# Optimization experiments

Measured on AMD Instinct MI355X. Metric: run time of the kernel, lower is better.

The kernel has to match this reference:

```python
import jax, jax.numpy as jnp
import numpy as np

N_TOKENS = 131072      # flattened batch of latents
EMBED_DIM = 64         # embedding_dim
NUM_CODES = 1024       # num_embeddings
COMMIT_COST = 0.25     # commitment_cost
EPS_NORM = 1e-12       # F.normalize eps


def _l2_normalize(x):
    # matches F.normalize(x, dim=1): x / max(||x||_2, eps)
    n = jnp.sqrt(jnp.sum(x * x, axis=1, keepdims=True))
    return x / jnp.maximum(n, EPS_NORM)


def setup_inputs() -> dict:
    key = jax.random.key(0)
    k_in, k_w = jax.random.split(key)
    inputs = jax.random.normal(k_in, (N_TOKENS, EMBED_DIM), dtype=jnp.float32)
    # codebook init: uniform(-1/K, 1/K), as in the torch module
    weight = jax.random.uniform(k_w, (NUM_CODES, EMBED_DIM), dtype=jnp.float32,
                                minval=-1.0 / NUM_CODES, maxval=1.0 / NUM_CODES)
    return {"inputs": inputs, "weight": weight}


def reference(inputs, weight):
    # Eval-mode forward of VectorQuantizer (EMA/anchor update is a training-only
    # in-place buffer mutation and is excluded from the functional reference).
    input_shape = inputs.shape
    d = weight.shape[1]
    flat = inputs.reshape(-1, d)                         # [N, D]

    normed_z = _l2_normalize(jax.lax.stop_gradient(flat))  # [N, D]
    normed_cb = _l2_normalize(weight)                       # [K, D]
    # distances = -cosine similarity; argmin picks closest code
    distances = -jnp.einsum('nd,kd->nk', normed_z, normed_cb)  # [N, K]
    idx = jnp.argmin(distances, axis=1)                         # [N]

    encodings = jax.nn.one_hot(idx, weight.shape[0], dtype=jnp.float32)  # [N, K]
    # one-hot @ weight == gather of codebook rows
    quantized = jnp.take(weight, idx, axis=0).reshape(input_shape)

    e_latent_loss = jnp.mean((jax.lax.stop_gradient(quantized) - inputs) ** 2)
    q_latent_loss = jnp.mean((quantized - jax.lax.stop_gradient(inputs)) ** 2)
    loss = q_latent_loss + COMMIT_COST * e_latent_loss

    # straight-through estimator
    quantized_st = inputs + jax.lax.stop_gradient(quantized - inputs)

    avg_probs = jnp.mean(encodings, axis=0)  # [K]
    perplexity = jnp.exp(-jnp.sum(avg_probs * jnp.log(avg_probs + 1e-10)))

    return loss, quantized_st, perplexity, encodings
```

## Files before the change

### kernel.cpp

```cpp
#include <hip/hip_runtime.h>
#include <math.h>

#define N_TOK 131072
#define DIM 64
#define KCODES 1024
#define TPB 128
#define TIE_EPS 1e-4f

typedef __attribute__((ext_vector_type(8))) short short8;
typedef __attribute__((ext_vector_type(4))) float float4v;

static __device__ inline unsigned short f2bf(float x) {
    unsigned u = __float_as_uint(x);
    unsigned r = (u + 0x7FFF + ((u >> 16) & 1)) >> 16;
    return (unsigned short)r;
}
static __device__ inline float bf2f(unsigned short b) {
    return __uint_as_float(((unsigned)b) << 16);
}

__global__ __launch_bounds__(64) void vq_prep(
    const float* __restrict__ w, unsigned short* __restrict__ bfrag_hi,
    unsigned short* __restrict__ bfrag_lo, double* __restrict__ inv_n64,
    float* __restrict__ nw, int* __restrict__ count, int* __restrict__ nflag,
    double* __restrict__ delta)
{
    int k = blockIdx.x;
    int d = threadIdx.x;
    float v = w[k * DIM + d];
    float s = v * v;
    #pragma unroll
    for (int off = 32; off; off >>= 1) s += __shfl_xor(s, off);
    float den = fmaxf(sqrtf(s), 1e-12f);
    float nv = v / den;
    unsigned short hi = f2bf(nv);
    unsigned short lo = f2bf(nv - bf2f(hi));

    int t  = k >> 4;
    int nl = k & 15;
    int s2 = d >> 5;
    int q  = (d >> 3) & 3;
    int j  = d & 7;
    int l  = nl + 16 * q;
    size_t pos = ((size_t)(t * 2 + s2) * 64 + l) * 8 + j;
    bfrag_hi[pos] = hi;
    bfrag_lo[pos] = lo;

    double vd = (double)v;
    double sd = vd * vd;
    #pragma unroll
    for (int off = 32; off; off >>= 1) sd += __shfl_xor(sd, off);
    if (d == 0) {
        inv_n64[k] = 1.0 / fmax(sqrt(sd), 1e-12);
        nw[k] = den;
    }
    if (k == 0) {
        for (int i = d; i < KCODES; i += 64) count[i] = 0;
        if (d == 0) { nflag[0] = 0; delta[0] = 0.0; }
    }
}

static __device__ inline void merge3(float& b, float& s, int& i, float ob, float os, int oi) {
    if (ob > b) { s = fmaxf(b, os); b = ob; i = oi; }
    else if (ob == b) { s = b; if (oi < i) i = oi; }
    else { s = fmaxf(s, ob); }
}

__global__ __launch_bounds__(256, 4) void vq_main(
    const float* __restrict__ inputs, const float* __restrict__ w,
    const unsigned short* __restrict__ bfrag_hi, const unsigned short* __restrict__ bfrag_lo,
    const float* __restrict__ nw, int* __restrict__ g_idx, int* __restrict__ count,
    double* __restrict__ partial, int* __restrict__ nflag, int* __restrict__ flags,
    float* __restrict__ out_q, float* __restrict__ out_enc)
{
    __shared__ int   s_idx[TPB];
    __shared__ float s_part[4];

    const int tid  = threadIdx.x;
    const int lane = tid & 63;
    const int wv   = tid >> 6;
    const int col  = lane & 15;
    const int quad = lane >> 4;
    const int n0   = blockIdx.x * TPB;

    short8 ah[2][2], al[2][2];
    float n2z[2];
    #pragma unroll
    for (int s = 0; s < 2; s++) {
        int m = n0 + wv * 32 + s * 16 + col;
        const float* zp = inputs + (size_t)m * DIM + quad * 8;
        float4 f0 = *(const float4*)zp;
        float4 f1 = *(const float4*)(zp + 4);
        float4 f2 = *(const float4*)(zp + 32);
        float4 f3 = *(const float4*)(zp + 36);
        float v[16] = {f0.x,f0.y,f0.z,f0.w, f1.x,f1.y,f1.z,f1.w,
                       f2.x,f2.y,f2.z,f2.w, f3.x,f3.y,f3.z,f3.w};
        float ss = 0.f;
        #pragma unroll
        for (int j = 0; j < 16; j++) ss += v[j] * v[j];
        ss += __shfl_xor(ss, 16);
        ss += __shfl_xor(ss, 32);
        n2z[s] = ss;
        float inv = 1.0f / fmaxf(sqrtf(ss), 1e-12f);
        #pragma unroll
        for (int j = 0; j < 8; j++) {
            float x0 = v[j] * inv;
            unsigned short h0 = f2bf(x0);
            ah[s][0][j] = (short)h0;
            al[s][0][j] = (short)f2bf(x0 - bf2f(h0));
            float x1 = v[8 + j] * inv;
            unsigned short h1 = f2bf(x1);
            ah[s][1][j] = (short)h1;
            al[s][1][j] = (short)f2bf(x1 - bf2f(h1));
        }
    }

    float* enc0 = out_enc + (size_t)n0 * KCODES;
    float* zp4  = enc0 + 2 + tid * 4;
    const float4 zero4 = {0.f, 0.f, 0.f, 0.f};

    float best[8], sec[8]; int bidx[8];
    #pragma unroll
    for (int i = 0; i < 8; i++) { best[i] = -1e30f; sec[i] = -1e30f; bidx[i] = 0x7fffffff; }

    const short8* bhp = (const short8*)bfrag_hi;
    const short8* blp = (const short8*)bfrag_lo;
    short8 c0h = bhp[lane], c1h = bhp[64 + lane];
    short8 c0l = blp[lane], c1l = blp[64 + lane];

    for (int t = 0; t < 64; t++) {
        int tn = (t < 63) ? (t + 1) : 63;
        size_t o = (size_t)(2 * tn) * 64 + lane;
        short8 p0h = bhp[o], p1h = bhp[o + 64];
        short8 p0l = blp[o], p1l = blp[o + 64];

        if (t < 63) {
            *(float4*)zp4 = zero4;
            *(float4*)(zp4 + KCODES) = zero4;
            zp4 += 2 * KCODES;
        }

        float4v acc0 = {0.f,0.f,0.f,0.f}, acc1 = {0.f,0.f,0.f,0.f};
        acc0 = __builtin_amdgcn_mfma_f32_16x16x32_bf16(ah[0][0], c0h, acc0, 0,0,0);
        acc1 = __builtin_amdgcn_mfma_f32_16x16x32_bf16(ah[1][0], c0h, acc1, 0,0,0);
        acc0 = __builtin_amdgcn_mfma_f32_16x16x32_bf16(al[0][0], c0h, acc0, 0,0,0);
        acc1 = __builtin_amdgcn_mfma_f32_16x16x32_bf16(al[1][0], c0h, acc1, 0,0,0);
        acc0 = __builtin_amdgcn_mfma_f32_16x16x32_bf16(ah[0][0], c0l, acc0, 0,0,0);
        acc1 = __builtin_amdgcn_mfma_f32_16x16x32_bf16(ah[1][0], c0l, acc1, 0,0,0);
        acc0 = __builtin_amdgcn_mfma_f32_16x16x32_bf16(ah[0][1], c1h, acc0, 0,0,0);
        acc1 = __builtin_amdgcn_mfma_f32_16x16x32_bf16(ah[1][1], c1h, acc1, 0,0,0);
        acc0 = __builtin_amdgcn_mfma_f32_16x16x32_bf16(al[0][1], c1h, acc0, 0,0,0);
        acc1 = __builtin_amdgcn_mfma_f32_16x16x32_bf16(al[1][1], c1h, acc1, 0,0,0);
        acc0 = __builtin_amdgcn_mfma_f32_16x16x32_bf16(ah[0][1], c1l, acc0, 0,0,0);
        acc1 = __builtin_amdgcn_mfma_f32_16x16x32_bf16(ah[1][1], c1l, acc1, 0,0,0);

        int k = t * 16 + col;
        #pragma unroll
        for (int i = 0; i < 4; i++) {
            float v0 = acc0[i];
            sec[i]  = __builtin_amdgcn_fmed3f(best[i], sec[i], v0);
            bool g0 = v0 > best[i];
            best[i] = fmaxf(best[i], v0);
            bidx[i] = g0 ? k : bidx[i];
            float v1 = acc1[i];
            sec[4+i]  = __builtin_amdgcn_fmed3f(best[4+i], sec[4+i], v1);
            bool g1 = v1 > best[4 + i];
            best[4 + i] = fmaxf(best[4 + i], v1);
            bidx[4 + i] = g1 ? k : bidx[4 + i];
        }
        c0h = p0h; c1h = p1h; c0l = p0l; c1l = p1l;
    }

    #pragma unroll
    for (int i = 126; i < 128; i++) {
        int q = i * 256 + tid;
        if (q < 32767) *(float4*)(enc0 + 2 + 4 * (size_t)q) = zero4;
    }
    if (tid == 0) {
        *(float2*)enc0 = make_float2(0.f, 0.f);
        *(float2*)(enc0 + (size_t)TPB * KCODES - 2) = make_float2(0.f, 0.f);
    }

    #pragma unroll
    for (int off = 1; off < 16; off <<= 1) {
        #pragma unroll
        for (int i = 0; i < 8; i++) {
            float ob = __shfl_xor(best[i], off);
            float os = __shfl_xor(sec[i], off);
            int   oi = __shfl_xor(bidx[i], off);
            merge3(best[i], sec[i], bidx[i], ob, os, oi);
        }
    }

    float lsum = 0.f;
    #pragma unroll
    for (int s = 0; s < 2; s++) {
        #pragma unroll
        for (int i = 0; i < 4; i++) {
            int r = s * 4 + i;
            float n2 = __shfl(n2z[s], quad * 4 + i);
            if (col == 0) {
                int u  = quad * 4 + i;
                int tl = wv * 32 + s * 16 + u;
                int k  = bidx[r];
                s_idx[tl] = k;
                g_idx[n0 + tl] = k;
                atomicAdd(&count[k], 1);
                if (best[r] - sec[r] < TIE_EPS) {
                    int p = atomicAdd(nflag, 1);
                    flags[p] = n0 + tl;
                }
                float nwk = nw[k];
                float zw  = best[r] * sqrtf(n2) * nwk;
                lsum += n2 - 2.f * zw + nwk * nwk;
            }
        }
    }
    lsum += __shfl_xor(lsum, 16);
    lsum += __shfl_xor(lsum, 32);
    if (lane == 0) s_part[wv] = lsum;
    __syncthreads();
    if (tid == 0)
        partial[blockIdx.x] = (double)(s_part[0] + s_part[1] + s_part[2] + s_part[3]);

    if (tid < TPB)
        out_enc[(size_t)(n0 + tid) * KCODES + s_idx[tid]] = 1.0f;

    const size_t qbase = (size_t)n0 * DIM;
    #pragma unroll 4
    for (int i2 = 0; i2 < 32; i2++) {
        int p = i2 * 256 + tid;
        int r = p >> 6, c = p & 63;
        int k = s_idx[r];
        out_q[qbase + p] = w[(size_t)k * DIM + c];
    }
}

__global__ __launch_bounds__(64) void vq_rescan(
    const float* __restrict__ inputs, const float* __restrict__ w,
    const double* __restrict__ inv_n64, const int* __restrict__ g_idx,
    const int* __restrict__ flags, const int* __restrict__ nflag,
    int* __restrict__ count, float* __restrict__ out_q,
    float* __restrict__ out_enc, double* __restrict__ delta)
{
    __shared__ double sz[64];
    int lane = threadIdx.x;
    int nf = nflag[0];
    for (int i = blockIdx.x; i < nf; i += gridDim.x) {
        int tok = flags[i];
        double zd = (double)inputs[(size_t)tok * DIM + lane];
        double ss = zd * zd;
        #pragma unroll
        for (int off = 32; off; off >>= 1) ss += __shfl_xor(ss, off);
        sz[lane] = zd / fmax(sqrt(ss), 1e-12);
        __syncthreads();
        double bv = -1e300; int bi = 0x7fffffff;
        for (int c = 0; c < 16; c++) {
            int k = c * 64 + lane;
            double invk = inv_n64[k];
            double dot = 0.0;
            #pragma unroll 8
            for (int d = 0; d < DIM; d++)
                dot += sz[d] * ((double)w[(size_t)k * DIM + d] * invk);
            if (dot > bv) { bv = dot; bi = k; }
        }
        #pragma unroll
        for (int off = 1; off < 64; off <<= 1) {
            double ov = __shfl_xor(bv, off);
            int   oi = __shfl_xor(bi, off);
            if (ov > bv || (ov == bv && oi < bi)) { bv = ov; bi = oi; }
        }
        int kold = g_idx[tok];
        if (bi != kold) {
            double wn = (double)w[(size_t)bi * DIM + lane];
            double wo = (double)w[(size_t)kold * DIM + lane];
            double zr = (double)inputs[(size_t)tok * DIM + lane];
            double a = wn * wn - wo * wo - 2.0 * zr * (wn - wo);
            #pragma unroll
            for (int off = 32; off; off >>= 1) a += __shfl_xor(a, off);
            out_q[(size_t)tok * DIM + lane] = (float)wn;
            if (lane == 0) {
                atomicAdd(&count[kold], -1);
                atomicAdd(&count[bi], 1);
                out_enc[(size_t)tok * KCODES + kold] = 0.f;
                out_enc[(size_t)tok * KCODES + bi]   = 1.f;
                atomicAdd(delta, a);
            }
        }
        __syncthreads();
    }
}

__global__ __launch_bounds__(256) void vq_final(
    const int* __restrict__ count, const double* __restrict__ partial,
    const double* __restrict__ delta, float* __restrict__ out_loss,
    float* __restrict__ out_perp)
{
    __shared__ double s1[256], s2[256];
    int tid = threadIdx.x;
    double lp = 0.0, ls = 0.0;
    for (int k = tid; k < KCODES; k += 256) {
        double p = (double)count[k] / (double)N_TOK;
        lp += p * log(p + 1e-10);
    }
    for (int i = tid; i < 1024; i += 256) ls += partial[i];
    s1[tid] = lp; s2[tid] = ls;
    __syncthreads();
    for (int st = 128; st; st >>= 1) {
        if (tid < st) { s1[tid] += s1[tid + st]; s2[tid] += s2[tid + st]; }
        __syncthreads();
    }
    if (tid == 0) {
        out_perp[0] = (float)exp(-s1[0]);
        out_loss[0] = (float)(1.25 * (s2[0] + delta[0]) / ((double)N_TOK * (double)DIM));
    }
}

extern "C" void kernel_launch(void* const* d_in, const int* in_sizes, int n_in,
                              void* d_out, int out_size, void* d_ws, size_t ws_size,
                              hipStream_t stream) {
    const float* inputs = (const float*)d_in[0];
    const float* weight = (const float*)d_in[1];
    float* out      = (float*)d_out;
    float* out_loss = out;
    float* out_q    = out + 1;
    float* out_perp = out + 1 + (size_t)N_TOK * DIM;
    float* out_enc  = out_perp + 1;

    char* ws = (char*)d_ws;
    unsigned short* bfrag_hi = (unsigned short*)ws;
    unsigned short* bfrag_lo = (unsigned short*)(ws + 131072);
    double* inv_n64 = (double*)(ws + 262144);
    float*  nw      = (float*)(ws + 270336);
    int*    g_idx   = (int*)(ws + 274432);
    int*    count   = (int*)(ws + 798720);
    double* partial = (double*)(ws + 802816);
    double* delta   = (double*)(ws + 811008);
    int*    nflag   = (int*)(ws + 811016);
    int*    flags   = (int*)(ws + 811020);

    vq_prep<<<KCODES, 64, 0, stream>>>(weight, bfrag_hi, bfrag_lo, inv_n64, nw,
                                       count, nflag, delta);
    vq_main<<<N_TOK / TPB, 256, 0, stream>>>(inputs, weight, bfrag_hi, bfrag_lo, nw,
                                             g_idx, count, partial, nflag, flags,
                                             out_q, out_enc);
    vq_rescan<<<256, 64, 0, stream>>>(inputs, weight, inv_n64, g_idx, flags, nflag,
                                      count, out_q, out_enc, delta);
    vq_final<<<1, 256, 0, stream>>>(count, partial, delta, out_loss, out_perp);
}
```

Baseline: 679.4 us.

## Split encodings zero-fill and quantized gather out of the main VQ kernel

Moves the 512 MB one-hot zero-fill out of the MFMA argmin kernel into a separate grid-stride zeroing kernel. The one-hot writes and the codebook-row gather for the quantized output move into a new scatter kernel that reads the stored indices. The aim is to stop the bandwidth-bound stores from interleaving with the compute loop and to let each phase run at its own efficiency. The cost is two extra launches and an extra read of g_idx, and the compute no longer overlaps the memory writes.

After: 790.8 us. +16.4%, slower.

```diff
diff --git a/kernel.cpp b/kernel.cpp
--- a/kernel.cpp
+++ b/kernel.cpp
@@ -60,6 +60,21 @@
     }
 }
 
+__global__ __launch_bounds__(256) void vq_zero(float* __restrict__ enc)
+{
+    const size_t NF4 = ((size_t)N_TOK * KCODES - 4) / 4;
+    float4* p = (float4*)(enc + 2);
+    const float4 z4 = {0.f, 0.f, 0.f, 0.f};
+    size_t i = (size_t)blockIdx.x * 256 + threadIdx.x;
+    const size_t stride = (size_t)gridDim.x * 256;
+    for (size_t j = i; j < NF4; j += stride) p[j] = z4;
+    if (i == 0) {
+        enc[0] = 0.f; enc[1] = 0.f;
+        enc[(size_t)N_TOK * KCODES - 2] = 0.f;
+        enc[(size_t)N_TOK * KCODES - 1] = 0.f;
+    }
+}
+
 static __device__ inline void merge3(float& b, float& s, int& i, float ob, float os, int oi) {
     if (ob > b) { s = fmaxf(b, os); b = ob; i = oi; }
     else if (ob == b) { s = b; if (oi < i) i = oi; }
@@ -67,13 +82,11 @@
 }
 
 __global__ __launch_bounds__(256, 4) void vq_main(
-    const float* __restrict__ inputs, const float* __restrict__ w,
+    const float* __restrict__ inputs,
     const unsigned short* __restrict__ bfrag_hi, const unsigned short* __restrict__ bfrag_lo,
     const float* __restrict__ nw, int* __restrict__ g_idx, int* __restrict__ count,
-    double* __restrict__ partial, int* __restrict__ nflag, int* __restrict__ flags,
-    float* __restrict__ out_q, float* __restrict__ out_enc)
-{
-    __shared__ int   s_idx[TPB];
+    double* __restrict__ partial, int* __restrict__ nflag, int* __restrict__ flags)
+{
     __shared__ float s_part[4];
 
     const int tid  = threadIdx.x;
@@ -115,10 +128,6 @@
         }
     }
 
-    float* enc0 = out_enc + (size_t)n0 * KCODES;
-    float* zp4  = enc0 + 2 + tid * 4;
-    const float4 zero4 = {0.f, 0.f, 0.f, 0.f};
-
     float best[8], sec[8]; int bidx[8];
     #pragma unroll
     for (int i = 0; i < 8; i++) { best[i] = -1e30f; sec[i] = -1e30f; bidx[i] = 0x7fffffff; }
@@ -133,12 +142,6 @@
         size_t o = (size_t)(2 * tn) * 64 + lane;
         short8 p0h = bhp[o], p1h = bhp[o + 64];
         short8 p0l = blp[o], p1l = blp[o + 64];
-
-        if (t < 63) {
-            *(float4*)zp4 = zero4;
-            *(float4*)(zp4 + KCODES) = zero4;
-            zp4 += 2 * KCODES;
-        }
 
         float4v acc0 = {0.f,0.f,0.f,0.f}, acc1 = {0.f,0.f,0.f,0.f};
         acc0 = __builtin_amdgcn_mfma_f32_16x16x32_bf16(ah[0][0], c0h, acc0, 0,0,0);
@@ -172,16 +175,6 @@
     }
 
     #pragma unroll
-    for (int i = 126; i < 128; i++) {
-        int q = i * 256 + tid;
-        if (q < 32767) *(float4*)(enc0 + 2 + 4 * (size_t)q) = zero4;
-    }
-    if (tid == 0) {
-        *(float2*)enc0 = make_float2(0.f, 0.f);
-        *(float2*)(enc0 + (size_t)TPB * KCODES - 2) = make_float2(0.f, 0.f);
-    }
-
-    #pragma unroll
     for (int off = 1; off < 16; off <<= 1) {
         #pragma unroll
         for (int i = 0; i < 8; i++) {
@@ -200,10 +193,8 @@
             int r = s * 4 + i;
             float n2 = __shfl(n2z[s], quad * 4 + i);
             if (col == 0) {
-                int u  = quad * 4 + i;
-                int tl = wv * 32 + s * 16 + u;
+                int tl = wv * 32 + s * 16 + quad * 4 + i;
                 int k  = bidx[r];
-                s_idx[tl] = k;
                 g_idx[n0 + tl] = k;
                 atomicAdd(&count[k], 1);
                 if (best[r] - sec[r] < TIE_EPS) {
@@ -222,18 +213,20 @@
     __syncthreads();
     if (tid == 0)
         partial[blockIdx.x] = (double)(s_part[0] + s_part[1] + s_part[2] + s_part[3]);
-
-    if (tid < TPB)
-        out_enc[(size_t)(n0 + tid) * KCODES + s_idx[tid]] = 1.0f;
-
-    const size_t qbase = (size_t)n0 * DIM;
-    #pragma unroll 4
-    for (int i2 = 0; i2 < 32; i2++) {
-        int p = i2 * 256 + tid;
-        int r = p >> 6, c = p & 63;
-        int k = s_idx[r];
-        out_q[qbase + p] = w[(size_t)k * DIM + c];
-    }
+}
+
+__global__ __launch_bounds__(256) void vq_scatter(
+    const float* __restrict__ w, const int* __restrict__ g_idx,
+    float* __restrict__ out_q, float* __restrict__ out_enc)
+{
+    int g  = blockIdx.x * 256 + threadIdx.x;
+    int n  = g >> 4;
+    int d4 = (g & 15) * 4;
+    int k  = g_idx[n];
+    float4 q = *(const float4*)&w[(size_t)k * DIM + d4];
+    size_t ob = (size_t)n * DIM + d4;
+    out_q[ob + 0] = q.x; out_q[ob + 1] = q.y; out_q[ob + 2] = q.z; out_q[ob + 3] = q.w;
+    if ((g & 15) == 0) out_enc[(size_t)n * KCODES + k] = 1.0f;
 }
 
 __global__ __launch_bounds__(64) void vq_rescan(
@@ -341,9 +334,10 @@
 
     vq_prep<<<KCODES, 64, 0, stream>>>(weight, bfrag_hi, bfrag_lo, inv_n64, nw,
                                        count, nflag, delta);
-    vq_main<<<N_TOK / TPB, 256, 0, stream>>>(inputs, weight, bfrag_hi, bfrag_lo, nw,
-                                             g_idx, count, partial, nflag, flags,
-                                             out_q, out_enc);
+    vq_zero<<<2048, 256, 0, stream>>>(out_enc);
+    vq_main<<<N_TOK / TPB, 256, 0, stream>>>(inputs, bfrag_hi, bfrag_lo, nw,
+                                             g_idx, count, partial, nflag, flags);
+    vq_scatter<<<(N_TOK * 16) / 256, 256, 0, stream>>>(weight, g_idx, out_q, out_enc);
     vq_rescan<<<256, 64, 0, stream>>>(inputs, weight, inv_n64, g_idx, flags, nflag,
                                       count, out_q, out_enc, delta);
     vq_final<<<1, 256, 0, stream>>>(count, partial, delta, out_loss, out_perp);
```

## Front-load one-hot zero stores, split rescan dot accumulators, widen rescan grid

Applied to the files above, without the earlier changes.

Moves a quarter of the one-hot encoding zero-fill ahead of the MFMA loop, overlapping it with input loads and normalization. The remaining zero stores are spread over the first 48 iterations instead of 63, and the tail fix-up is adjusted to match. The rescan kernel's double-precision dot product is split into four independent accumulators to shorten the dependency chain, and its grid grows from 256 to 2048 blocks. This front-loads store traffic and adds more blocks in the rescan pass, at the cost of extra launch and scheduling overhead when few tokens are flagged.

Result: no change. 675.3 us (-0.6%).

```diff
diff --git a/kernel.cpp b/kernel.cpp
--- a/kernel.cpp
+++ b/kernel.cpp
@@ -83,18 +83,33 @@
     const int quad = lane >> 4;
     const int n0   = blockIdx.x * TPB;
 
-    short8 ah[2][2], al[2][2];
-    float n2z[2];
+    float4 f[2][4];
     #pragma unroll
     for (int s = 0; s < 2; s++) {
         int m = n0 + wv * 32 + s * 16 + col;
         const float* zp = inputs + (size_t)m * DIM + quad * 8;
-        float4 f0 = *(const float4*)zp;
-        float4 f1 = *(const float4*)(zp + 4);
-        float4 f2 = *(const float4*)(zp + 32);
-        float4 f3 = *(const float4*)(zp + 36);
-        float v[16] = {f0.x,f0.y,f0.z,f0.w, f1.x,f1.y,f1.z,f1.w,
-                       f2.x,f2.y,f2.z,f2.w, f3.x,f3.y,f3.z,f3.w};
+        f[s][0] = *(const float4*)zp;
+        f[s][1] = *(const float4*)(zp + 4);
+        f[s][2] = *(const float4*)(zp + 32);
+        f[s][3] = *(const float4*)(zp + 36);
+    }
+
+    float* enc0 = out_enc + (size_t)n0 * KCODES;
+    const float4 zero4 = {0.f, 0.f, 0.f, 0.f};
+    #pragma unroll 8
+    for (int i = 0; i < 32; i++) {
+        int p = i * 256 + tid;
+        *(float4*)(enc0 + 2 + 4 * (size_t)p) = zero4;
+    }
+
+    short8 ah[2][2], al[2][2];
+    float n2z[2];
+    #pragma unroll
+    for (int s = 0; s < 2; s++) {
+        float v[16] = {f[s][0].x,f[s][0].y,f[s][0].z,f[s][0].w,
+                       f[s][1].x,f[s][1].y,f[s][1].z,f[s][1].w,
+                       f[s][2].x,f[s][2].y,f[s][2].z,f[s][2].w,
+                       f[s][3].x,f[s][3].y,f[s][3].z,f[s][3].w};
         float ss = 0.f;
         #pragma unroll
         for (int j = 0; j < 16; j++) ss += v[j] * v[j];
@@ -115,10 +130,6 @@
         }
     }
 
-    float* enc0 = out_enc + (size_t)n0 * KCODES;
-    float* zp4  = enc0 + 2 + tid * 4;
-    const float4 zero4 = {0.f, 0.f, 0.f, 0.f};
-
     float best[8], sec[8]; int bidx[8];
     #pragma unroll
     for (int i = 0; i < 8; i++) { best[i] = -1e30f; sec[i] = -1e30f; bidx[i] = 0x7fffffff; }
@@ -127,6 +138,8 @@
     const short8* blp = (const short8*)bfrag_lo;
     short8 c0h = bhp[lane], c1h = bhp[64 + lane];
     short8 c0l = blp[lane], c1l = blp[64 + lane];
+
+    float* zp4 = enc0 + 2 + (size_t)(32 * 256 + tid) * 4;
 
     for (int t = 0; t < 64; t++) {
         int tn = (t < 63) ? (t + 1) : 63;
@@ -134,9 +147,10 @@
         short8 p0h = bhp[o], p1h = bhp[o + 64];
         short8 p0l = blp[o], p1l = blp[o + 64];
 
-        if (t < 63) {
+        if (t < 48) {
+            int p = (32 + 2 * t) * 256 + tid;
             *(float4*)zp4 = zero4;
-            *(float4*)(zp4 + KCODES) = zero4;
+            if (p + 256 < 32767) *(float4*)(zp4 + KCODES) = zero4;
             zp4 += 2 * KCODES;
         }
 
@@ -171,14 +185,13 @@
         c0h = p0h; c1h = p1h; c0l = p0l; c1l = p1l;
     }
 
-    #pragma unroll
-    for (int i = 126; i < 128; i++) {
-        int q = i * 256 + tid;
-        if (q < 32767) *(float4*)(enc0 + 2 + 4 * (size_t)q) = zero4;
-    }
     if (tid == 0) {
         *(float2*)enc0 = make_float2(0.f, 0.f);
         *(float2*)(enc0 + (size_t)TPB * KCODES - 2) = make_float2(0.f, 0.f);
+    }
+    if (tid == 255) {
+        float* q = enc0 + 2 + (size_t)32767 * 4;
+        q[0] = 0.f; q[1] = 0.f; q[2] = 0.f; q[3] = 0.f;
     }
 
     #pragma unroll
@@ -200,8 +213,7 @@
             int r = s * 4 + i;
             float n2 = __shfl(n2z[s], quad * 4 + i);
             if (col == 0) {
-                int u  = quad * 4 + i;
-                int tl = wv * 32 + s * 16 + u;
+                int tl = wv * 32 + s * 16 + quad * 4 + i;
                 int k  = bidx[r];
                 s_idx[tl] = k;
                 g_idx[n0 + tl] = k;
@@ -258,10 +270,16 @@
         for (int c = 0; c < 16; c++) {
             int k = c * 64 + lane;
             double invk = inv_n64[k];
-            double dot = 0.0;
-            #pragma unroll 8
-            for (int d = 0; d < DIM; d++)
-                dot += sz[d] * ((double)w[(size_t)k * DIM + d] * invk);
+            const float* wr = w + (size_t)k * DIM;
+            double d0 = 0.0, d1 = 0.0, d2 = 0.0, d3 = 0.0;
+            #pragma unroll
+            for (int d = 0; d < DIM; d += 4) {
+                d0 += sz[d + 0] * ((double)wr[d + 0] * invk);
+                d1 += sz[d + 1] * ((double)wr[d + 1] * invk);
+                d2 += sz[d + 2] * ((double)wr[d + 2] * invk);
+                d3 += sz[d + 3] * ((double)wr[d + 3] * invk);
+            }
+            double dot = (d0 + d1) + (d2 + d3);
             if (dot > bv) { bv = dot; bi = k; }
         }
         #pragma unroll
@@ -344,7 +362,7 @@
     vq_main<<<N_TOK / TPB, 256, 0, stream>>>(inputs, weight, bfrag_hi, bfrag_lo, nw,
                                              g_idx, count, partial, nflag, flags,
                                              out_q, out_enc);
-    vq_rescan<<<256, 64, 0, stream>>>(inputs, weight, inv_n64, g_idx, flags, nflag,
-                                      count, out_q, out_enc, delta);
+    vq_rescan<<<2048, 64, 0, stream>>>(inputs, weight, inv_n64, g_idx, flags, nflag,
+                                       count, out_q, out_enc, delta);
     vq_final<<<1, 256, 0, stream>>>(count, partial, delta, out_loss, out_perp);
 }
```
